# Kernel tuning notes

Hardware: AMD Instinct MI355X
Metric: run time of the kernel (lower is better)

Reference implementation:

```python
import jax, jax.numpy as jnp
import numpy as np

B, N, T_IN, T_OUT, NF = 8, 1024, 10, 20, 1
WIDTH, K_SPACE, M_TIME, KNN = 32, 16, 4, 8


def setup_inputs() -> dict:
    key = jax.random.key(0)
    ks = jax.random.split(key, 10)
    scale = 1.0 / (WIDTH * WIDTH)
    return {
        "x": jax.random.normal(ks[0], (B, N, T_IN, NF), dtype=jnp.float32),
        "pos": jax.random.uniform(ks[1], (B, N, 2), dtype=jnp.float32),
        "Wp": 0.05 * jax.random.normal(ks[2], (T_IN * NF + 3, WIDTH), dtype=jnp.float32),
        "bp": jnp.zeros((WIDTH,), jnp.float32),
        "fw_r": scale * jax.random.uniform(ks[3], (4, WIDTH, WIDTH, K_SPACE, M_TIME), dtype=jnp.float32),
        "fw_i": scale * jax.random.uniform(ks[4], (4, WIDTH, WIDTH, K_SPACE, M_TIME), dtype=jnp.float32),
        "cw": 0.05 * jax.random.normal(ks[5], (4, WIDTH, WIDTH), dtype=jnp.float32),
        "cb": jnp.zeros((4, WIDTH), jnp.float32),
        "q1w": 0.05 * jax.random.normal(ks[6], (WIDTH, 128), dtype=jnp.float32),
        "q1b": jnp.zeros((128,), jnp.float32),
        "q2w": 0.05 * jax.random.normal(ks[7], (128, NF), dtype=jnp.float32),
        "q2b": jnp.zeros((NF,), jnp.float32),
    }


def _graph_laplacian(feat):
    # feat: [B, C, N] -> symmetric-normalized kNN graph Laplacian [B, N, N]
    xp = jnp.transpose(feat, (0, 2, 1))                      # [B, N, C]
    sq = jnp.sum(xp * xp, axis=-1)                           # [B, N]
    D2 = sq[:, :, None] + sq[:, None, :] - 2.0 * jnp.einsum('bnc,bmc->bnm', xp, xp)
    D2 = jnp.maximum(D2, 0.0)
    D2s = jnp.where(D2 > 0.0, D2, 1.0)                       # safe sqrt (zero grad at 0)
    Dm = jnp.where(D2 > 0.0, jnp.sqrt(D2s), 0.0)             # [B, N, N] pairwise distances
    k = min(KNN, Dm.shape[1] - 1)
    _, idx = jax.lax.top_k(-Dm, k)                           # [B, N, k] nearest (incl. self)
    sigma = jnp.mean(Dm, axis=(-2, -1), keepdims=True)       # [B, 1, 1]
    vals = jnp.exp(-jnp.take_along_axis(Dm, idx, axis=-1) / (sigma ** 2))
    b = jnp.arange(Dm.shape[0])[:, None, None]
    n = jnp.arange(Dm.shape[1])[None, :, None]
    A = jnp.zeros_like(Dm).at[b, n, idx].set(vals)
    A = 0.5 * (A + jnp.swapaxes(A, -2, -1))
    deg = jnp.sum(A, axis=-1)                                # [B, N]
    I = jnp.eye(Dm.shape[1], dtype=A.dtype)
    L = deg[:, :, None] * I - A
    dinv = 1.0 / jnp.sqrt(deg + 1e-6)
    return dinv[:, :, None] * L * dinv[:, None, :]


def _fourier_layer(h, Wc):
    # h: [B, C, N, T]; Wc: [C, C, K_SPACE, M_TIME] complex64
    Bx, C, Nn, T = h.shape
    L = _graph_laplacian(h[..., 0])
    ev, evec = jnp.linalg.eigh(L)
    order = jnp.argsort(ev, axis=-1)[..., :K_SPACE]          # [B, K]
    order_b = jnp.broadcast_to(order[:, None, :], (Bx, Nn, K_SPACE))
    basis = jnp.take_along_axis(evec, order_b, axis=-1)      # [B, N, K] real spectral basis
    xs = jnp.einsum('bnk,bcnt->bckt', basis, h)              # project onto K spatial modes
    xf = jnp.fft.rfft(xs, axis=-1)                           # [B, C, K, T//2+1]
    of = jnp.einsum('bixt,ioxt->boxt', xf[..., :M_TIME], Wc)
    pad = xf.shape[-1] - M_TIME
    of_full = jnp.concatenate([of, jnp.zeros(of.shape[:-1] + (pad,), of.dtype)], axis=-1)
    os = jnp.fft.irfft(of_full, n=T, axis=-1)                # back to time, real
    return jnp.einsum('bnk,bckt->bcnt', basis, os)


def _forward(x, pos, Wp, bp, fw_r, fw_i, cw, cb, q1w, q1b, q2w, q2b):
    Bx, Nn = x.shape[0], x.shape[1]
    t = jnp.linspace(0.0, 1.0, T_OUT + T_IN)[T_IN:]          # [T_OUT]
    xb = jnp.broadcast_to(x.reshape(Bx, Nn, 1, T_IN * NF), (Bx, Nn, T_OUT, T_IN * NF))
    pb = jnp.broadcast_to(pos[:, :, None, :], (Bx, Nn, T_OUT, pos.shape[-1]))
    tg = jnp.broadcast_to(t[None, None, :, None], (Bx, Nn, T_OUT, 1))
    h = jnp.concatenate([xb, pb, tg], axis=-1) @ Wp + bp     # [B, N, T_out, width]
    h = jnp.transpose(h, (0, 3, 1, 2))                       # [B, width, N, T_out]
    Wc = (fw_r + 1j * fw_i).astype(jnp.complex64)            # [4, C, C, K, MT]
    for i in range(4):
        h1 = _fourier_layer(h, Wc[i])
        h2 = jnp.einsum('oi,bint->bont', cw[i], h) + cb[i][None, :, None, None]
        h = h1 + h2
        if i < 3:
            h = jax.nn.gelu(h, approximate=False)
    h = jnp.transpose(h, (0, 2, 3, 1))                       # [B, N, T_out, width]
    h = jax.nn.gelu(h @ q1w + q1b, approximate=False)
    return h @ q2w + q2b                                     # [B, N, T_out, NF]


def reference(x, pos, Wp, bp, fw_r, fw_i, cw, cb, q1w, q1b, q2w, q2b):
    return _forward(x, pos, Wp, bp, fw_r, fw_i, cw, cb, q1w, q1b, q2w, q2b)
```

## Files before the change

kernel.cpp:

```cpp
#include <hip/hip_runtime.h>

#define NB 8
#define NN 1024
#define NC 32
#define NT 20
#define NTI 10
#define NM 32
#define NK 16
#define NMT 4
#define WE 64
#define NQ 128
#define GNN (NB*NN)
#define RSL 24
#define PTC 16
#define PSEG 16

__device__ __forceinline__ float gelu_f(float x){
  return 0.5f * x * (1.0f + erff(x * 0.70710678118654752f));
}
__device__ __forceinline__ unsigned wanghash(unsigned s){
  s = (s ^ 61u) ^ (s >> 16); s *= 9u; s ^= s >> 4; s *= 0x27d4eb2du; s ^= s >> 15;
  return s;
}

__global__ void k_build_h0(const float* __restrict__ x, const float* __restrict__ pos,
                           const float* __restrict__ Wp, const float* __restrict__ bp,
                           float* __restrict__ h, float* __restrict__ feat){
  int idx = blockIdx.x*256 + threadIdx.x;
  if (idx >= NB*NN*NT*NC) return;
  int c = idx & (NC-1);
  int t = (idx/NC) % NT;
  int n = (idx/(NC*NT)) & (NN-1);
  int b = idx/(NC*NT*NN);
  const float* xr = x + (b*NN + n)*NTI;
  float acc = bp[c];
  #pragma unroll
  for (int i=0;i<NTI;i++) acc += xr[i]*Wp[i*NC+c];
  acc += pos[(b*NN+n)*2+0]*Wp[10*NC+c];
  acc += pos[(b*NN+n)*2+1]*Wp[11*NC+c];
  float tv = (float)(10+t) * (1.0f/29.0f);
  acc += tv*Wp[12*NC+c];
  h[idx] = acc;
  if (t == 0) feat[(((size_t)b*NC + c)<<10) + n] = acc;
}

__global__ __launch_bounds__(256) void k_dist_knn(const float* __restrict__ h,
                           const float* __restrict__ feat,
                           float* __restrict__ knnd, int* __restrict__ knni,
                           double* __restrict__ sig, int* __restrict__ cnt){
  __shared__ float fr_s[4][NC];
  int wave = threadIdx.x >> 6;
  int lane = threadIdx.x & 63;
  int b  = blockIdx.x & 7;
  int rg = blockIdx.x >> 3;
  int row = (b<<10) + rg*4 + wave;
  if (threadIdx.x < 4*NC){
    int w = threadIdx.x >> 5, c = threadIdx.x & 31;
    int rr = (b<<10) + rg*4 + w;
    fr_s[w][c] = h[((size_t)rr*NT)*NC + c];
  }
  __syncthreads();
  float d8[8]; int i8[8];
  #pragma unroll
  for (int j=0;j<8;j++){ d8[j]=1e30f; i8[j]=0x3fffffff; }
  double ssum = 0.0;
  const float* fc_b = feat + (((size_t)b*NC)<<10);
  for (int tile=0; tile<8; tile++){
    int m = tile*128 + lane;
    float d2a = 0.f, d2b = 0.f;
    #pragma unroll 8
    for (int c=0;c<NC;c++){
      float fc = fr_s[wave][c];
      const float* fp = fc_b + ((size_t)c<<10) + m;
      float dfa = fc - fp[0];
      float dfb = fc - fp[64];
      d2a += dfa*dfa; d2b += dfb*dfb;
    }
    float da = sqrtf(d2a);
    ssum += (double)da;
    if (da < d8[7] || (da == d8[7] && m < i8[7])){
      d8[7] = da; i8[7] = m;
      #pragma unroll
      for (int j=6;j>=0;j--){
        bool sw = (d8[j+1] < d8[j]) || (d8[j+1]==d8[j] && i8[j+1]<i8[j]);
        if (sw){ float td=d8[j]; d8[j]=d8[j+1]; d8[j+1]=td;
                 int ti=i8[j]; i8[j]=i8[j+1]; i8[j+1]=ti; }
      }
    }
    int m2 = m + 64;
    float db = sqrtf(d2b);
    ssum += (double)db;
    if (db < d8[7] || (db == d8[7] && m2 < i8[7])){
      d8[7] = db; i8[7] = m2;
      #pragma unroll
      for (int j=6;j>=0;j--){
        bool sw = (d8[j+1] < d8[j]) || (d8[j+1]==d8[j] && i8[j+1]<i8[j]);
        if (sw){ float td=d8[j]; d8[j]=d8[j+1]; d8[j+1]=td;
                 int ti=i8[j]; i8[j]=i8[j+1]; i8[j+1]=ti; }
      }
    }
  }
  #pragma unroll
  for (int off=32; off>0; off>>=1) ssum += __shfl_down(ssum, off);
  if (lane==0){ atomicAdd(&sig[b], ssum); cnt[row] = 8; }
  int ptr = 0;
  for (int sel=0; sel<8; sel++){
    float dv = 1e30f; int iv = 0x3fffffff;
    #pragma unroll
    for (int j=0;j<8;j++) if (j==ptr){ dv=d8[j]; iv=i8[j]; }
    float bd = dv; int bi = iv;
    #pragma unroll
    for (int off=32; off>0; off>>=1){
      float od = __shfl_xor(bd, off);
      int oi = __shfl_xor(bi, off);
      if (od < bd || (od == bd && oi < bi)){ bd = od; bi = oi; }
    }
    if (dv == bd && iv == bi) ptr++;
    if (lane == sel){ knnd[row*8+sel] = bd; knni[row*8+sel] = bi; }
  }
}

__global__ void k_build_ell(const float* __restrict__ knnd, const int* __restrict__ knni,
                            const double* __restrict__ sig, int* __restrict__ cnt,
                            unsigned short* __restrict__ ecolT, float* __restrict__ evalT){
  int row = blockIdx.x*256 + threadIdx.x;
  if (row >= NB*NN) return;
  int b = row >> 10;
  float sigma = (float)(sig[b] * (1.0/((double)NN*(double)NN)));
  float s2 = sigma*sigma;
  int rloc = row & (NN-1);
  #pragma unroll
  for (int j=0;j<8;j++){
    float d = knnd[row*8+j];
    int m = knni[row*8+j];
    float v = 0.5f * expf(-d/s2);
    ecolT[(size_t)j*GNN + row] = (unsigned short)m;
    evalT[(size_t)j*GNN + row] = v;
    int grow = (b<<10) + m;
    int p = atomicAdd(&cnt[grow], 1);
    if (p < WE){ ecolT[(size_t)p*GNN + grow] = (unsigned short)rloc;
                 evalT[(size_t)p*GNN + grow] = v; }
  }
}

__global__ void k_degnorm(const int* __restrict__ cnt, const float* __restrict__ evalT,
                          float* __restrict__ deg, float* __restrict__ dinv){
  int row = blockIdx.x*256 + threadIdx.x;
  if (row >= NB*NN) return;
  int c = cnt[row]; if (c > WE) c = WE;
  float s = 0.f;
  for (int j=0;j<c;j++) s += evalT[(size_t)j*GNN + row];
  deg[row] = s;
  dinv[row] = 1.0f/sqrtf(s + 1e-6f);
}

__global__ void k_normell(const int* __restrict__ cnt, const unsigned short* __restrict__ ecolT,
                          float* __restrict__ evalT, const float* __restrict__ deg,
                          const float* __restrict__ dinv, float* __restrict__ dval){
  int row = blockIdx.x*256 + threadIdx.x;
  if (row >= NB*NN) return;
  int b = row >> 10;
  const float* dv = dinv + (b<<10);
  float di = dinv[row];
  int c = cnt[row]; if (c > WE) c = WE;
  for (int j=0;j<c;j++){
    int col = ecolT[(size_t)j*GNN + row];
    evalT[(size_t)j*GNN + row] = evalT[(size_t)j*GNN + row] * (di * dv[col]);
  }
  dval[row] = di*di*deg[row];
}

__global__ void k_initX(const float* __restrict__ deg, float* __restrict__ X, float* __restrict__ aint){
  int idx = blockIdx.x*256+threadIdx.x;
  if (idx >= NB*NM*NN) return;
  int n = idx & (NN-1);
  int j = (idx >> 10) & (NM-1);
  int b = idx >> 15;
  float v;
  if (j == 0) v = sqrtf(deg[(b<<10)+n] + 1e-6f);
  else {
    unsigned hsh = wanghash((unsigned)idx * 2654435761u + 12345u);
    v = ((hsh >> 8) * (1.0f/16777216.0f)) - 0.5f;
  }
  X[idx] = v;
  if (n == 0 && j == 1) aint[b] = 1.0f;
}

__global__ __launch_bounds__(512) void k_cheb(const int* __restrict__ cnt,
                        const unsigned short* __restrict__ ecolT,
                        const float* __restrict__ evalT, const float* __restrict__ dval,
                        float* __restrict__ X, const float* __restrict__ aint, int ndeg){
  __shared__ float bufA[NN];
  __shared__ float bufB[NN];
  int b = blockIdx.x & 7;
  int col = blockIdx.x >> 3;
  float a = aint[b];
  const float bhi = 2.0005f;
  float e  = 0.5f*(bhi - a);
  float cc = 0.5f*(bhi + a);
  float inv_e = 1.0f/e;
  const int rowbase = b << 10;
  float* Xc = X + ((size_t)b*NM + col)*NN;
  for (int n=threadIdx.x; n<NN; n+=512) bufA[n] = Xc[n];
  int r0 = threadIdx.x, r1 = threadIdx.x + 512;
  int c0 = cnt[rowbase+r0]; if (c0 > WE) c0 = WE;
  int c1 = cnt[rowbase+r1]; if (c1 > WE) c1 = WE;
  float dv0 = dval[rowbase+r0];
  float dv1 = dval[rowbase+r1];
  float ev0[RSL], ev1[RSL];
  int   ic0[RSL], ic1[RSL];
  #pragma unroll
  for (int j=0;j<RSL;j++){
    ic0[j] = (j<c0)? (int)ecolT[(size_t)j*GNN + rowbase + r0] : 0;
    ev0[j] = (j<c0)? evalT[(size_t)j*GNN + rowbase + r0] : 0.f;
    ic1[j] = (j<c1)? (int)ecolT[(size_t)j*GNN + rowbase + r1] : 0;
    ev1[j] = (j<c1)? evalT[(size_t)j*GNN + rowbase + r1] : 0.f;
  }
  int e0 = c0 - RSL; if (e0 < 0) e0 = 0;
  int e1 = c1 - RSL; if (e1 < 0) e1 = 0;
  int emax = (e0 > e1)? e0 : e1;
  const unsigned short* pe0 = ecolT + (size_t)RSL*GNN + rowbase + r0;
  const unsigned short* pe1 = ecolT + (size_t)RSL*GNN + rowbase + r1;
  const float* pv0 = evalT + (size_t)RSL*GNN + rowbase + r0;
  const float* pv1 = evalT + (size_t)RSL*GNN + rowbase + r1;
  __syncthreads();
  float* cur = bufA; float* prv = bufB;
  for (int k=0;k<ndeg;k++){
    float f = (k==0)? inv_e : 2.0f*inv_e;
    float x0 = cur[r0], x1 = cur[r1];
    float acc0 = dv0*x0, acc1 = dv1*x1;
    #pragma unroll
    for (int j=0;j<RSL;j++){
      acc0 -= ev0[j]*cur[ic0[j]];
      acc1 -= ev1[j]*cur[ic1[j]];
    }
    for (int j=0;j<emax;j++){
      if (j < e0) acc0 -= pv0[(size_t)j*GNN] * cur[pe0[(size_t)j*GNN]];
      if (j < e1) acc1 -= pv1[(size_t)j*GNN] * cur[pe1[(size_t)j*GNN]];
    }
    float n0 = f*(acc0 - cc*x0);
    float n1 = f*(acc1 - cc*x1);
    if (k > 0){ n0 -= prv[r0]; n1 -= prv[r1]; }
    prv[r0] = n0; prv[r1] = n1;
    float* t_ = cur; cur = prv; prv = t_;
    __syncthreads();
  }
  for (int n=threadIdx.x; n<NN; n+=512) Xc[n] = cur[n];
}

__global__ void k_gram(const float* __restrict__ A, const float* __restrict__ Bm,
                       double* __restrict__ G){
  __shared__ float ai[NN];
  __shared__ double pd[NM][8];
  int b = blockIdx.x & 7, i = blockIdx.x >> 3;
  const float* Ac = A + ((size_t)b*NM + i)*NN;
  for (int n=threadIdx.x; n<NN; n+=256) ai[n] = Ac[n];
  __syncthreads();
  int j = threadIdx.x & 31, seg = threadIdx.x >> 5;
  const float* Bc = Bm + ((size_t)b*NM + j)*NN + seg*128;
  const float* as = ai + seg*128;
  double s = 0.0;
  for (int n=0;n<128;n++) s += (double)as[n]*(double)Bc[n];
  pd[j][seg] = s;
  __syncthreads();
  if (threadIdx.x < NM){
    double t = 0.0;
    #pragma unroll
    for (int q=0;q<8;q++) t += pd[threadIdx.x][q];
    G[((size_t)b*NM + i)*NM + threadIdx.x] = t;
  }
}

__global__ __launch_bounds__(256) void k_cholapply(const double* __restrict__ G,
                        const float* __restrict__ Xin, float* __restrict__ Xout,
                        float* __restrict__ aint, int reset){
  __shared__ double L[NM][NM];
  __shared__ double Ri[NM][NM];
  int b = blockIdx.x >> 2;
  int quarter = blockIdx.x & 3;
  int tid = threadIdx.x;
  for (int idx=tid; idx<NM*NM; idx+=256) L[idx>>5][idx&31] = G[(size_t)b*NM*NM + idx];
  __syncthreads();
  for (int k=0;k<NM;k++){
    if (tid == 0){
      double orig = L[k][k];
      double s = orig;
      for (int p=0;p<k;p++) s -= L[k][p]*L[k][p];
      double floorv = orig*1e-15; if (floorv < 1e-30) floorv = 1e-30;
      if (s < floorv) s = floorv;
      L[k][k] = sqrt(s);
    }
    __syncthreads();
    if (tid > k && tid < NM){
      double s = L[tid][k];
      for (int p=0;p<k;p++) s -= L[tid][p]*L[k][p];
      L[tid][k] = s / L[k][k];
    }
    __syncthreads();
  }
  if (tid < NM){
    int j = tid;
    Ri[j][j] = 1.0 / L[j][j];
    for (int i=j-1;i>=0;i--){
      double s = 0.0;
      for (int k2=i+1;k2<=j;k2++) s += L[k2][i]*Ri[k2][j];
      Ri[i][j] = -s / L[i][i];
    }
  }
  __syncthreads();
  int n = quarter*256 + tid;
  float xv[NM];
  #pragma unroll
  for (int j=0;j<NM;j++) xv[j] = Xin[((size_t)b*NM + j)*NN + n];
  for (int jn=0;jn<NM;jn++){
    double acc = 0.0;
    for (int j=0;j<=jn;j++) acc += (double)xv[j] * Ri[j][jn];
    Xout[((size_t)b*NM + jn)*NN + n] = (float)acc;
  }
  if (reset && quarter==0 && tid==0) aint[b] = 0.02f;
}

__global__ __launch_bounds__(256) void k_spmv_gersh(const int* __restrict__ cnt,
                        const unsigned short* __restrict__ ecolT,
                        const float* __restrict__ evalT, const float* __restrict__ dval,
                        const float* __restrict__ X, float* __restrict__ aint){
  __shared__ float xc[NN];
  __shared__ float yc[NN];
  __shared__ double pd[NM][8];
  int b = blockIdx.x & 7, j = blockIdx.x >> 3;
  const float* Xc = X + ((size_t)b*NM + j)*NN;
  for (int n=threadIdx.x; n<NN; n+=256) xc[n] = Xc[n];
  __syncthreads();
  int rowbase = b << 10;
  for (int r=threadIdx.x; r<NN; r+=256){
    int c = cnt[rowbase+r]; if (c > WE) c = WE;
    float acc = dval[rowbase+r]*xc[r];
    const unsigned short* pe = ecolT + rowbase + r;
    const float* pv = evalT + rowbase + r;
    for (int jj=0;jj<c;jj++){
      acc -= pv[0]*xc[pe[0]];
      pe += GNN; pv += GNN;
    }
    yc[r] = acc;
  }
  __syncthreads();
  int i = threadIdx.x >> 3, seg = threadIdx.x & 7;
  const float* Xi = X + ((size_t)b*NM + i)*NN + seg*128;
  const float* ys = yc + seg*128;
  double s = 0.0;
  for (int k=0;k<128;k++) s += (double)Xi[k]*(double)ys[k];
  pd[i][seg] = s;
  __syncthreads();
  if (threadIdx.x < NM){
    double g = 0.0;
    #pragma unroll
    for (int q=0;q<8;q++) g += pd[threadIdx.x][q];
    double contrib = (threadIdx.x==j)? g : fabs(g);
    #pragma unroll
    for (int off=16; off>0; off>>=1) contrib += __shfl_down(contrib, off, 32);
    if (threadIdx.x == 0){
      float av = (float)contrib*1.02f + 1e-4f;
      av = fminf(fmaxf(av, 0.02f), 1.5f);
      atomicMax((unsigned int*)&aint[b], __float_as_uint(av));
    }
  }
}

__global__ __launch_bounds__(256) void k_spmv_gram(const int* __restrict__ cnt,
                        const unsigned short* __restrict__ ecolT,
                        const float* __restrict__ evalT, const float* __restrict__ dval,
                        const float* __restrict__ X, double* __restrict__ G){
  __shared__ float xc[NN];
  __shared__ float yc[NN];
  __shared__ double pd[NM][8];
  int b = blockIdx.x & 7, j = blockIdx.x >> 3;
  const float* Xc = X + ((size_t)b*NM + j)*NN;
  for (int n=threadIdx.x; n<NN; n+=256) xc[n] = Xc[n];
  __syncthreads();
  int rowbase = b << 10;
  for (int r=threadIdx.x; r<NN; r+=256){
    int c = cnt[rowbase+r]; if (c > WE) c = WE;
    float acc = dval[rowbase+r]*xc[r];
    const unsigned short* pe = ecolT + rowbase + r;
    const float* pv = evalT + rowbase + r;
    for (int jj=0;jj<c;jj++){
      acc -= pv[0]*xc[pe[0]];
      pe += GNN; pv += GNN;
    }
    yc[r] = acc;
  }
  __syncthreads();
  int i = threadIdx.x >> 3, seg = threadIdx.x & 7;
  const float* Xi = X + ((size_t)b*NM + i)*NN + seg*128;
  const float* ys = yc + seg*128;
  double s = 0.0;
  for (int k=0;k<128;k++) s += (double)Xi[k]*(double)ys[k];
  pd[i][seg] = s;
  __syncthreads();
  if (threadIdx.x < NM){
    double g = 0.0;
    #pragma unroll
    for (int q=0;q<8;q++) g += pd[threadIdx.x][q];
    G[((size_t)b*NM + j)*NM + threadIdx.x] = g;
  }
}

__global__ __launch_bounds__(256) void k_jacobi(const double* __restrict__ Gd,
                        float* __restrict__ Vpf, int sweeps){
  __shared__ float S[NM][NM];
  __shared__ float V[NM][NM];
  __shared__ float cs_[16], sn_[16];
  __shared__ int pp_[16], qq_[16];
  __shared__ int perm[NM];
  int b = blockIdx.x, l = threadIdx.x;
  for (int idx=l; idx<NM*NM; idx+=256){
    int i = idx>>5, j = idx&31;
    S[i][j] = (float)(0.5*(Gd[(size_t)b*NM*NM + i*NM + j] + Gd[(size_t)b*NM*NM + j*NM + i]));
    V[i][j] = (i==j)? 1.0f : 0.0f;
  }
  __syncthreads();
  for (int sw=0; sw<sweeps; sw++){
    for (int r=0; r<31; r++){
      if (l < 16){
        int p, q;
        if (l == 0){ p = r; q = 31; }
        else { p = (r + l) % 31; q = (r + 31 - l) % 31; }
        if (p > q){ int t_=p; p=q; q=t_; }
        float apq = S[p][q];
        float c = 1.0f, s = 0.0f;
        if (fabsf(apq) > 1e-30f){
          float tau = (S[q][q] - S[p][p]) / (2.0f*apq);
          float tt = (tau >= 0.f ? 1.0f : -1.0f) / (fabsf(tau) + sqrtf(1.0f + tau*tau));
          c = 1.0f/sqrtf(1.0f + tt*tt); s = tt*c;
        }
        cs_[l]=c; sn_[l]=s; pp_[l]=p; qq_[l]=q;
      }
      __syncthreads();
      for (int tsk=l; tsk<512; tsk+=256){
        int i = tsk >> 4, kk = tsk & 15;
        int p = pp_[kk], q = qq_[kk];
        float c = cs_[kk], s = sn_[kk];
        float sp = S[i][p], sq = S[i][q];
        S[i][p] = c*sp - s*sq; S[i][q] = s*sp + c*sq;
        float vp = V[i][p], vq = V[i][q];
        V[i][p] = c*vp - s*vq; V[i][q] = s*vp + c*vq;
      }
      __syncthreads();
      for (int tsk=l; tsk<512; tsk+=256){
        int jc = tsk >> 4, kk = tsk & 15;
        int p = pp_[kk], q = qq_[kk];
        float c = cs_[kk], s = sn_[kk];
        float sp = S[p][jc], sq = S[q][jc];
        S[p][jc] = c*sp - s*sq; S[q][jc] = s*sp + c*sq;
      }
      __syncthreads();
    }
  }
  if (l < NM){
    float v = S[l][l];
    int rank = 0;
    #pragma unroll
    for (int i=0;i<NM;i++){
      float vi = S[i][i];
      rank += (vi < v || (vi == v && i < l)) ? 1 : 0;
    }
    perm[rank] = l;
  }
  __syncthreads();
  for (int idx=l; idx<NM*NM; idx+=256){
    int i = idx>>5, j = idx&31;
    Vpf[(size_t)b*NM*NM + i*NM + j] = V[i][perm[j]];
  }
}

__global__ __launch_bounds__(256) void k_applyVf(const float* __restrict__ Xin,
                        const float* __restrict__ Vpf, float* __restrict__ Xout){
  __shared__ float Ms[NM*NM];
  int b = blockIdx.x >> 2;
  int n = (blockIdx.x & 3)*256 + threadIdx.x;
  for (int idx=threadIdx.x; idx<NM*NM; idx+=256) Ms[idx] = Vpf[(size_t)b*NM*NM + idx];
  __syncthreads();
  float xv[NM];
  #pragma unroll
  for (int j=0;j<NM;j++) xv[j] = Xin[((size_t)b*NM + j)*NN + n];
  #pragma unroll
  for (int jn=0;jn<NM;jn++){
    float acc = 0.f;
    #pragma unroll
    for (int j=0;j<NM;j++) acc += xv[j]*Ms[j*NM + jn];
    Xout[((size_t)b*NM + jn)*NN + n] = acc;
  }
}

__global__ __launch_bounds__(256) void k_project(const float* __restrict__ X, const float* __restrict__ h,
                          float* __restrict__ xs){
  __shared__ float Xs[NK][NN];
  __shared__ float red[PSEG][NK][PTC+1];
  int b = blockIdx.x & 7;
  int chunk = blockIdx.x >> 3;
  int tc0 = chunk * PTC;
  for (int idx=threadIdx.x; idx<NK*NN; idx+=256){
    int k = idx >> 10, n = idx & (NN-1);
    Xs[k][n] = X[((size_t)b*NM + k)*NN + n];
  }
  __syncthreads();
  int tcl = threadIdx.x & (PTC-1);
  int seg = threadIdx.x >> 4;
  const float* hb = h + (size_t)b*NN*NT*NC + tc0 + tcl;
  float acc[NK];
  #pragma unroll
  for (int k=0;k<NK;k++) acc[k]=0.f;
  int n0 = seg*(NN/PSEG);
  for (int n=n0; n<n0+(NN/PSEG); n++){
    float v = hb[(size_t)n*NT*NC];
    #pragma unroll
    for (int k=0;k<NK;k++) acc[k] += Xs[k][n]*v;
  }
  #pragma unroll
  for (int k=0;k<NK;k++) red[seg][k][tcl] = acc[k];
  __syncthreads();
  int k = threadIdx.x >> 4;
  int t2 = threadIdx.x & (PTC-1);
  float s = 0.f;
  #pragma unroll
  for (int q=0;q<PSEG;q++) s += red[q][k][t2];
  xs[((size_t)b*NK + k)*NT*NC + tc0 + t2] = s;
}

__global__ __launch_bounds__(64) void k_timefilter(const float* __restrict__ xs, const float* __restrict__ fwr,
                             const float* __restrict__ fwi, float* __restrict__ osb, int layer){
  __shared__ float xst[NT*NC];
  __shared__ float xfr[NC][NMT];
  __shared__ float xfi[NC][NMT];
  int b = blockIdx.x >> 4, k = blockIdx.x & 15;
  const float* xin = xs + ((size_t)b*NK + k)*NT*NC;
  for (int idx=threadIdx.x; idx<NT*NC; idx+=64) xst[idx] = xin[idx];
  __syncthreads();
  int l = threadIdx.x;
  if (l < NC){
    float ar0=0,ar1=0,ar2=0,ar3=0, ai1=0,ai2=0,ai3=0;
    for (int t=0;t<NT;t++){
      float v = xst[t*NC + l];
      float w1 = 0.31415926535897932f * (float)t;
      ar0 += v;
      ar1 += v*cosf(w1);       ai1 -= v*sinf(w1);
      ar2 += v*cosf(2.f*w1);   ai2 -= v*sinf(2.f*w1);
      ar3 += v*cosf(3.f*w1);   ai3 -= v*sinf(3.f*w1);
    }
    xfr[l][0]=ar0; xfi[l][0]=0.f;
    xfr[l][1]=ar1; xfi[l][1]=ai1;
    xfr[l][2]=ar2; xfi[l][2]=ai2;
    xfr[l][3]=ar3; xfi[l][3]=ai3;
  }
  __syncthreads();
  if (l < NC){
    int o = l;
    float ofr[NMT], ofi[NMT];
    #pragma unroll
    for (int f=0; f<NMT; f++){ ofr[f]=0.f; ofi[f]=0.f; }
    for (int i=0;i<NC;i++){
      size_t wbase = ((((size_t)layer*NC + i)*NC + o)*NK + k)*NMT;
      #pragma unroll
      for (int f=0; f<NMT; f++){
        float wr = fwr[wbase+f], wi2 = fwi[wbase+f];
        float xr = xfr[i][f], xi = xfi[i][f];
        ofr[f] += xr*wr - xi*wi2;
        ofi[f] += xr*wi2 + xi*wr;
      }
    }
    float* outp = osb + ((size_t)b*NK + k)*NT*NC;
    for (int t=0;t<NT;t++){
      float w1 = 0.31415926535897932f * (float)t;
      float acc = ofr[0];
      acc += 2.f*(ofr[1]*cosf(w1)     - ofi[1]*sinf(w1));
      acc += 2.f*(ofr[2]*cosf(2.f*w1) - ofi[2]*sinf(2.f*w1));
      acc += 2.f*(ofr[3]*cosf(3.f*w1) - ofi[3]*sinf(3.f*w1));
      outp[t*NC + o] = acc * 0.05f;
    }
  }
}

__global__ __launch_bounds__(256) void k_update(const float* __restrict__ X, const float* __restrict__ osb,
                         const float* __restrict__ h, const float* __restrict__ cw,
                         const float* __restrict__ cb, float* __restrict__ hout,
                         float* __restrict__ feat, int layer){
  __shared__ float os_s[NK*NT*NC];
  __shared__ float cwT[NC*NC];
  __shared__ float Xl[NK][32];
  __shared__ float cbs[NC];
  int b = blockIdx.x & 7;
  int n0 = (blockIdx.x >> 3)*32;
  for (int idx=threadIdx.x; idx<NK*NT*NC; idx+=256) os_s[idx] = osb[(size_t)b*NK*NT*NC + idx];
  for (int idx=threadIdx.x; idx<NC*NC; idx+=256){
    int o = idx/NC, i = idx%NC;
    cwT[i*NC + o] = cw[((size_t)layer*NC + o)*NC + i];
  }
  if (threadIdx.x < NC) cbs[threadIdx.x] = cb[layer*NC + threadIdx.x];
  for (int idx=threadIdx.x; idx<NK*32; idx+=256){
    int k = idx >> 5, nl = idx & 31;
    Xl[k][nl] = X[((size_t)b*NM + k)*NN + n0 + nl];
  }
  __syncthreads();
  for (int tsk=threadIdx.x; tsk<32*NT; tsk+=256){
    int t = tsk % NT, nl = tsk / NT;
    int n = n0 + nl;
    const float* hr = h + (((size_t)b*NN + n)*NT + t)*NC;
    float acc[NC];
    #pragma unroll
    for (int o=0;o<NC;o++) acc[o] = cbs[o];
    #pragma unroll
    for (int k=0;k<NK;k++){
      float xv = Xl[k][nl];
      const float* osr = os_s + (k*NT + t)*NC;
      #pragma unroll
      for (int o=0;o<NC;o++) acc[o] += xv*osr[o];
    }
    for (int i=0;i<NC;i++){
      float hv = hr[i];
      const float* cwr = cwT + i*NC;
      #pragma unroll
      for (int o=0;o<NC;o++) acc[o] += hv*cwr[o];
    }
    float* outp = hout + (((size_t)b*NN + n)*NT + t)*NC;
    if (layer < 3){
      #pragma unroll
      for (int o=0;o<NC;o++){
        float v = gelu_f(acc[o]);
        outp[o] = v;
        if (t == 0) feat[(((size_t)b*NC + o)<<10) + n] = v;
      }
    } else {
      #pragma unroll
      for (int o=0;o<NC;o++){
        outp[o] = acc[o];
        if (t == 0) feat[(((size_t)b*NC + o)<<10) + n] = acc[o];
      }
    }
  }
}

__global__ __launch_bounds__(256) void k_head(const float* __restrict__ h, const float* __restrict__ q1w,
                       const float* __restrict__ q1b, const float* __restrict__ q2w,
                       const float* __restrict__ q2b, float* __restrict__ out){
  __shared__ float w1[NC*NQ];
  __shared__ float b1[NQ], w2[NQ];
  for (int idx=threadIdx.x; idx<NC*NQ; idx+=256) w1[idx] = q1w[idx];
  if (threadIdx.x < NQ){ b1[threadIdx.x] = q1b[threadIdx.x]; w2[threadIdx.x] = q2w[threadIdx.x]; }
  __syncthreads();
  int idx = blockIdx.x*256 + threadIdx.x;
  if (idx >= NB*NN*NT) return;
  const float* hr = h + (size_t)idx*NC;
  float hv[NC];
  #pragma unroll
  for (int i=0;i<NC;i++) hv[i] = hr[i];
  float res = q2b[0];
  for (int j=0;j<NQ;j++){
    float z = b1[j];
    #pragma unroll
    for (int i=0;i<NC;i++) z += hv[i]*w1[i*NQ + j];
    res += gelu_f(z)*w2[j];
  }
  out[idx] = res;
}

extern "C" void kernel_launch(void* const* d_in, const int* in_sizes, int n_in,
                              void* d_out, int out_size, void* d_ws, size_t ws_size,
                              hipStream_t stream){
  (void)in_sizes; (void)n_in; (void)out_size;
  const float* x   = (const float*)d_in[0];
  const float* pos = (const float*)d_in[1];
  const float* Wp  = (const float*)d_in[2];
  const float* bp  = (const float*)d_in[3];
  const float* fwr = (const float*)d_in[4];
  const float* fwi = (const float*)d_in[5];
  const float* cw  = (const float*)d_in[6];
  const float* cb  = (const float*)d_in[7];
  const float* q1w = (const float*)d_in[8];
  const float* q1b = (const float*)d_in[9];
  const float* q2w = (const float*)d_in[10];
  const float* q2b = (const float*)d_in[11];

  char* p = (char*)d_ws;
  auto take = [&](size_t bytes)->void*{
    void* r = (void*)p;
    p += (bytes + 255) & ~(size_t)255;
    return r;
  };
  float*  hA    = (float*) take(sizeof(float)*NB*NN*NT*NC);
  float*  hB    = (float*) take(sizeof(float)*NB*NN*NT*NC);
  float*  featb = (float*) take(sizeof(float)*NB*NC*NN);
  float*  knnd  = (float*) take(sizeof(float)*NB*NN*8);
  int*    knni  = (int*)   take(sizeof(int)*NB*NN*8);
  double* sig   = (double*)take(sizeof(double)*NB);
  int*    cntb  = (int*)   take(sizeof(int)*NB*NN);
  unsigned short* ecolT = (unsigned short*) take(sizeof(unsigned short)*(size_t)GNN*WE);
  float*  evalT = (float*) take(sizeof(float)*(size_t)GNN*WE);
  float*  deg   = (float*) take(sizeof(float)*NB*NN);
  float*  dinv  = (float*) take(sizeof(float)*NB*NN);
  float*  dval  = (float*) take(sizeof(float)*NB*NN);
  float*  Xb    = (float*) take(sizeof(float)*NB*NM*NN);
  float*  Yb    = (float*) take(sizeof(float)*NB*NM*NN);
  double* Gd    = (double*)take(sizeof(double)*NB*NM*NM);
  float*  Vpf   = (float*) take(sizeof(float)*NB*NM*NM);
  float*  aint  = (float*) take(sizeof(float)*NB);
  float*  xs    = (float*) take(sizeof(float)*NB*NK*NT*NC);
  float*  osb   = (float*) take(sizeof(float)*NB*NK*NT*NC);
  if ((size_t)(p - (char*)d_ws) > ws_size) return;

  k_build_h0<<<(NB*NN*NT*NC+255)/256, 256, 0, stream>>>(x, pos, Wp, bp, hA, featb);

  float* hcur = hA; float* hnext = hB;
  for (int layer=0; layer<4; layer++){
    hipMemsetAsync(sig, 0, sizeof(double)*NB, stream);
    k_dist_knn<<<NB*NN/4, 256, 0, stream>>>(hcur, featb, knnd, knni, sig, cntb);
    k_build_ell<<<NB*NN/256, 256, 0, stream>>>(knnd, knni, sig, cntb, ecolT, evalT);
    k_degnorm<<<NB*NN/256, 256, 0, stream>>>(cntb, evalT, deg, dinv);
    k_normell<<<NB*NN/256, 256, 0, stream>>>(cntb, ecolT, evalT, deg, dinv, dval);
    k_initX<<<NB*NM*NN/256, 256, 0, stream>>>(deg, Xb, aint);
    float* cur = Xb; float* oth = Yb;
    k_cheb<<<NB*NM, 512, 0, stream>>>(cntb, ecolT, evalT, dval, cur, aint, 24);
    k_gram<<<NB*NM, 256, 0, stream>>>(cur, cur, Gd);
    k_cholapply<<<NB*4, 256, 0, stream>>>(Gd, cur, oth, aint, 1);
    { float* t_ = cur; cur = oth; oth = t_; }
    k_spmv_gersh<<<NB*NM, 256, 0, stream>>>(cntb, ecolT, evalT, dval, cur, aint);
    k_cheb<<<NB*NM, 512, 0, stream>>>(cntb, ecolT, evalT, dval, cur, aint, 32);
    k_gram<<<NB*NM, 256, 0, stream>>>(cur, cur, Gd);
    k_cholapply<<<NB*4, 256, 0, stream>>>(Gd, cur, oth, aint, 0);
    { float* t_ = cur; cur = oth; oth = t_; }
    k_spmv_gram<<<NB*NM, 256, 0, stream>>>(cntb, ecolT, evalT, dval, cur, Gd);
    k_jacobi<<<NB, 256, 0, stream>>>(Gd, Vpf, 1);
    k_applyVf<<<NB*4, 256, 0, stream>>>(cur, Vpf, oth);
    { float* t_ = cur; cur = oth; oth = t_; }

    k_project<<<NB*40, 256, 0, stream>>>(cur, hcur, xs);
    k_timefilter<<<NB*NK, 64, 0, stream>>>(xs, fwr, fwi, osb, layer);
    k_update<<<NB*32, 256, 0, stream>>>(cur, osb, hcur, cw, cb, hnext, featb, layer);
    { float* t_ = hcur; hcur = hnext; hnext = t_; }
  }
  k_head<<<(NB*NN*NT+255)/256, 256, 0, stream>>>(hcur, q1w, q1b, q2w, q2b, (float*)d_out);
}
```

Baseline: 3.045 ms.

## Split distance and kNN into tiled distance kernel plus selection kernel

Adds a tiled pairwise-distance kernel that writes the full [B,N,N] distance matrix to workspace using 64x64 shared-memory tiles with 4x4 register blocking. A separate kNN kernel then streams each row to do top-8 selection and sum the values for sigma. This falls back to the fused kernel if the workspace is too small. Separately, cholapply runs 64-thread blocks over 16 segments per batch and jacobi runs 64-thread blocks, trading a larger block count for narrower blocks, with extra global memory traffic from the 32MB distance buffer.

```diff
diff --git a/kernel.cpp b/kernel.cpp
--- a/kernel.cpp
+++ b/kernel.cpp
@@ -42,6 +42,110 @@
   acc += tv*Wp[12*NC+c];
   h[idx] = acc;
   if (t == 0) feat[(((size_t)b*NC + c)<<10) + n] = acc;
+}
+
+__global__ __launch_bounds__(256) void k_dist(const float* __restrict__ feat,
+                          float* __restrict__ D){
+  __shared__ float frow[NC][64];
+  __shared__ float fcol[NC][64];
+  int b = blockIdx.x & 7;
+  int t = blockIdx.x >> 3;
+  int r0 = (t >> 4) * 64;
+  int m0 = (t & 15) * 64;
+  const float* fb = feat + (((size_t)b*NC)<<10);
+  #pragma unroll
+  for (int it=0; it<8; it++){
+    int idx = it*256 + threadIdx.x;
+    int c = idx >> 6, j = idx & 63;
+    frow[c][j] = fb[((size_t)c<<10) + r0 + j];
+    fcol[c][j] = fb[((size_t)c<<10) + m0 + j];
+  }
+  __syncthreads();
+  int rq = (threadIdx.x >> 4) << 2;
+  int mq = (threadIdx.x & 15) << 2;
+  float acc[4][4];
+  #pragma unroll
+  for (int i=0;i<4;i++)
+    #pragma unroll
+    for (int j=0;j<4;j++) acc[i][j] = 0.f;
+  #pragma unroll 8
+  for (int c=0;c<NC;c++){
+    float rv[4], cv[4];
+    #pragma unroll
+    for (int i=0;i<4;i++) rv[i] = frow[c][rq+i];
+    #pragma unroll
+    for (int j=0;j<4;j++) cv[j] = fcol[c][mq+j];
+    #pragma unroll
+    for (int i=0;i<4;i++)
+      #pragma unroll
+      for (int j=0;j<4;j++){ float df = rv[i]-cv[j]; acc[i][j] += df*df; }
+  }
+  #pragma unroll
+  for (int i=0;i<4;i++){
+    float4 o;
+    o.x = sqrtf(acc[i][0]); o.y = sqrtf(acc[i][1]);
+    o.z = sqrtf(acc[i][2]); o.w = sqrtf(acc[i][3]);
+    *(float4*)&D[(((size_t)(b<<10) + r0 + rq + i)<<10) + m0 + mq] = o;
+  }
+}
+
+__global__ __launch_bounds__(256) void k_knn(const float* __restrict__ D,
+                           float* __restrict__ knnd, int* __restrict__ knni,
+                           double* __restrict__ sig, int* __restrict__ cnt){
+  int wave = threadIdx.x >> 6;
+  int lane = threadIdx.x & 63;
+  int b  = blockIdx.x & 7;
+  int rg = blockIdx.x >> 3;
+  int row = (b<<10) + rg*4 + wave;
+  const float* Dr = D + ((size_t)row << 10);
+  float d8[8]; int i8[8];
+  #pragma unroll
+  for (int j=0;j<8;j++){ d8[j]=1e30f; i8[j]=0x3fffffff; }
+  double ssum = 0.0;
+  for (int tile=0; tile<8; tile++){
+    int m = tile*128 + lane;
+    float da = Dr[m];
+    float db = Dr[m+64];
+    ssum += (double)da;
+    if (da < d8[7] || (da == d8[7] && m < i8[7])){
+      d8[7] = da; i8[7] = m;
+      #pragma unroll
+      for (int j=6;j>=0;j--){
+        bool sw = (d8[j+1] < d8[j]) || (d8[j+1]==d8[j] && i8[j+1]<i8[j]);
+        if (sw){ float td=d8[j]; d8[j]=d8[j+1]; d8[j+1]=td;
+                 int ti=i8[j]; i8[j]=i8[j+1]; i8[j+1]=ti; }
+      }
+    }
+    int m2 = m + 64;
+    ssum += (double)db;
+    if (db < d8[7] || (db == d8[7] && m2 < i8[7])){
+      d8[7] = db; i8[7] = m2;
+      #pragma unroll
+      for (int j=6;j>=0;j--){
+        bool sw = (d8[j+1] < d8[j]) || (d8[j+1]==d8[j] && i8[j+1]<i8[j]);
+        if (sw){ float td=d8[j]; d8[j]=d8[j+1]; d8[j+1]=td;
+                 int ti=i8[j]; i8[j]=i8[j+1]; i8[j+1]=ti; }
+      }
+    }
+  }
+  #pragma unroll
+  for (int off=32; off>0; off>>=1) ssum += __shfl_down(ssum, off);
+  if (lane==0){ atomicAdd(&sig[b], ssum); cnt[row] = 8; }
+  int ptr = 0;
+  for (int sel=0; sel<8; sel++){
+    float dv = 1e30f; int iv = 0x3fffffff;
+    #pragma unroll
+    for (int j=0;j<8;j++) if (j==ptr){ dv=d8[j]; iv=i8[j]; }
+    float bd = dv; int bi = iv;
+    #pragma unroll
+    for (int off=32; off>0; off>>=1){
+      float od = __shfl_xor(bd, off);
+      int oi = __shfl_xor(bi, off);
+      if (od < bd || (od == bd && oi < bi)){ bd = od; bi = oi; }
+    }
+    if (dv == bd && iv == bi) ptr++;
+    if (lane == sel){ knnd[row*8+sel] = bd; knni[row*8+sel] = bi; }
+  }
 }
 
 __global__ __launch_bounds__(256) void k_dist_knn(const float* __restrict__ h,
@@ -271,15 +375,15 @@
   }
 }
 
-__global__ __launch_bounds__(256) void k_cholapply(const double* __restrict__ G,
+__global__ __launch_bounds__(64) void k_cholapply(const double* __restrict__ G,
                         const float* __restrict__ Xin, float* __restrict__ Xout,
                         float* __restrict__ aint, int reset){
   __shared__ double L[NM][NM];
   __shared__ double Ri[NM][NM];
-  int b = blockIdx.x >> 2;
-  int quarter = blockIdx.x & 3;
+  int b = blockIdx.x >> 4;
+  int seg = blockIdx.x & 15;
   int tid = threadIdx.x;
-  for (int idx=tid; idx<NM*NM; idx+=256) L[idx>>5][idx&31] = G[(size_t)b*NM*NM + idx];
+  for (int idx=tid; idx<NM*NM; idx+=64) L[idx>>5][idx&31] = G[(size_t)b*NM*NM + idx];
   __syncthreads();
   for (int k=0;k<NM;k++){
     if (tid == 0){
@@ -308,7 +412,7 @@
     }
   }
   __syncthreads();
-  int n = quarter*256 + tid;
+  int n = seg*64 + tid;
   float xv[NM];
   #pragma unroll
   for (int j=0;j<NM;j++) xv[j] = Xin[((size_t)b*NM + j)*NN + n];
@@ -317,7 +421,7 @@
     for (int j=0;j<=jn;j++) acc += (double)xv[j] * Ri[j][jn];
     Xout[((size_t)b*NM + jn)*NN + n] = (float)acc;
   }
-  if (reset && quarter==0 && tid==0) aint[b] = 0.02f;
+  if (reset && seg==0 && tid==0) aint[b] = 0.02f;
 }
 
 __global__ __launch_bounds__(256) void k_spmv_gersh(const int* __restrict__ cnt,
@@ -405,7 +509,7 @@
   }
 }
 
-__global__ __launch_bounds__(256) void k_jacobi(const double* __restrict__ Gd,
+__global__ __launch_bounds__(64) void k_jacobi(const double* __restrict__ Gd,
                         float* __restrict__ Vpf, int sweeps){
   __shared__ float S[NM][NM];
   __shared__ float V[NM][NM];
@@ -413,7 +517,7 @@
   __shared__ int pp_[16], qq_[16];
   __shared__ int perm[NM];
   int b = blockIdx.x, l = threadIdx.x;
-  for (int idx=l; idx<NM*NM; idx+=256){
+  for (int idx=l; idx<NM*NM; idx+=64){
     int i = idx>>5, j = idx&31;
     S[i][j] = (float)(0.5*(Gd[(size_t)b*NM*NM + i*NM + j] + Gd[(size_t)b*NM*NM + j*NM + i]));
     V[i][j] = (i==j)? 1.0f : 0.0f;
@@ -436,7 +540,7 @@
         cs_[l]=c; sn_[l]=s; pp_[l]=p; qq_[l]=q;
       }
       __syncthreads();
-      for (int tsk=l; tsk<512; tsk+=256){
+      for (int tsk=l; tsk<512; tsk+=64){
         int i = tsk >> 4, kk = tsk & 15;
         int p = pp_[kk], q = qq_[kk];
         float c = cs_[kk], s = sn_[kk];
@@ -446,7 +550,7 @@
         V[i][p] = c*vp - s*vq; V[i][q] = s*vp + c*vq;
       }
       __syncthreads();
-      for (int tsk=l; tsk<512; tsk+=256){
+      for (int tsk=l; tsk<512; tsk+=64){
         int jc = tsk >> 4, kk = tsk & 15;
         int p = pp_[kk], q = qq_[kk];
         float c = cs_[kk], s = sn_[kk];
@@ -467,7 +571,7 @@
     perm[rank] = l;
   }
   __syncthreads();
-  for (int idx=l; idx<NM*NM; idx+=256){
+  for (int idx=l; idx<NM*NM; idx+=64){
     int i = idx>>5, j = idx&31;
     Vpf[(size_t)b*NM*NM + i*NM + j] = V[i][perm[j]];
   }
@@ -706,13 +810,24 @@
   float*  xs    = (float*) take(sizeof(float)*NB*NK*NT*NC);
   float*  osb   = (float*) take(sizeof(float)*NB*NK*NT*NC);
   if ((size_t)(p - (char*)d_ws) > ws_size) return;
+  float* Dbuf = nullptr;
+  {
+    size_t used = (size_t)(p - (char*)d_ws);
+    size_t needD = ((sizeof(float)*(size_t)GNN*NN) + 255) & ~(size_t)255;
+    if (used + needD <= ws_size) Dbuf = (float*)take(sizeof(float)*(size_t)GNN*NN);
+  }
 
   k_build_h0<<<(NB*NN*NT*NC+255)/256, 256, 0, stream>>>(x, pos, Wp, bp, hA, featb);
 
   float* hcur = hA; float* hnext = hB;
   for (int layer=0; layer<4; layer++){
     hipMemsetAsync(sig, 0, sizeof(double)*NB, stream);
-    k_dist_knn<<<NB*NN/4, 256, 0, stream>>>(hcur, featb, knnd, knni, sig, cntb);
+    if (Dbuf){
+      k_dist<<<NB*256, 256, 0, stream>>>(featb, Dbuf);
+      k_knn<<<NB*NN/4, 256, 0, stream>>>(Dbuf, knnd, knni, sig, cntb);
+    } else {
+      k_dist_knn<<<NB*NN/4, 256, 0, stream>>>(hcur, featb, knnd, knni, sig, cntb);
+    }
     k_build_ell<<<NB*NN/256, 256, 0, stream>>>(knnd, knni, sig, cntb, ecolT, evalT);
     k_degnorm<<<NB*NN/256, 256, 0, stream>>>(cntb, evalT, deg, dinv);
     k_normell<<<NB*NN/256, 256, 0, stream>>>(cntb, ecolT, evalT, deg, dinv, dval);
@@ -720,15 +835,15 @@
     float* cur = Xb; float* oth = Yb;
     k_cheb<<<NB*NM, 512, 0, stream>>>(cntb, ecolT, evalT, dval, cur, aint, 24);
     k_gram<<<NB*NM, 256, 0, stream>>>(cur, cur, Gd);
-    k_cholapply<<<NB*4, 256, 0, stream>>>(Gd, cur, oth, aint, 1);
+    k_cholapply<<<NB*16, 64, 0, stream>>>(Gd, cur, oth, aint, 1);
     { float* t_ = cur; cur = oth; oth = t_; }
     k_spmv_gersh<<<NB*NM, 256, 0, stream>>>(cntb, ecolT, evalT, dval, cur, aint);
     k_cheb<<<NB*NM, 512, 0, stream>>>(cntb, ecolT, evalT, dval, cur, aint, 32);
     k_gram<<<NB*NM, 256, 0, stream>>>(cur, cur, Gd);
-    k_cholapply<<<NB*4, 256, 0, stream>>>(Gd, cur, oth, aint, 0);
+    k_cholapply<<<NB*16, 64, 0, stream>>>(Gd, cur, oth, aint, 0);
     { float* t_ = cur; cur = oth; oth = t_; }
     k_spmv_gram<<<NB*NM, 256, 0, stream>>>(cntb, ecolT, evalT, dval, cur, Gd);
-    k_jacobi<<<NB, 256, 0, stream>>>(Gd, Vpf, 1);
+    k_jacobi<<<NB, 64, 0, stream>>>(Gd, Vpf, 1);
     k_applyVf<<<NB*4, 256, 0, stream>>>(cur, Vpf, oth);
     { float* t_ = cur; cur = oth; oth = t_; }
 
```

After: 3.082 ms. Within noise of the previous version (+1.2%).
